# Performance work log

Measured on AMD Instinct MI355X. Metric: run time of the kernel, lower is better.

Reference implementation:

```python
import jax, jax.numpy as jnp
import numpy as np

B, S, N, F, H, G, O, P = 32, 12, 2048, 1, 128, 64, 1, 3


def setup_inputs() -> dict:
    key = jax.random.key(0)
    ks = jax.random.split(key, 12)
    x = jax.random.normal(ks[0], (B, S, N, F), jnp.float32)
    # row-normalized random adjacency (dense, as the module uses a dense adj)
    adj = jax.random.uniform(ks[1], (N, N), jnp.float32)
    adj = adj / jnp.sum(adj, axis=1, keepdims=True)
    s = 0.05
    return {
        "x": x,
        "adj": adj,
        "W_g1": jax.random.normal(ks[2], (F, G), jnp.float32) * s,
        "b_g1": jnp.zeros((G,), jnp.float32),
        "W_g2": jax.random.normal(ks[3], (G, H), jnp.float32) * s,
        "b_g2": jnp.zeros((H,), jnp.float32),
        "W_ih": jax.random.normal(ks[4], (H, 3 * H), jnp.float32) * s,
        "W_hh": jax.random.normal(ks[5], (H, 3 * H), jnp.float32) * s,
        "b_ih": jnp.zeros((3 * H,), jnp.float32),
        "b_hh": jnp.zeros((3 * H,), jnp.float32),
        "W_fc": jax.random.normal(ks[6], (H, O), jnp.float32) * s,
        "b_fc": jnp.zeros((O,), jnp.float32),
        "pred_len": P,
    }


def _tgcn_cell(xt, h, adj, W_g1, b_g1, W_g2, b_g2, W_ih, W_hh, b_ih, b_hh):
    # 2-layer GCN: relu(A X W1 + b1) -> A H1 W2 + b2
    # compute X@W first (F, G small), then propagate with dense adj
    h1 = jax.nn.relu(jnp.einsum('mn,bng->bmg', adj, xt @ W_g1) + b_g1)  # (B,N,G)
    xg = jnp.einsum('mn,bnh->bmh', adj, h1 @ W_g2) + b_g2              # (B,N,H)
    # standard GRU cell (gate order r, z, n)
    gx = xg @ W_ih + b_ih                                              # (B,N,3H)
    gh = h @ W_hh + b_hh
    rx, zx, nx = jnp.split(gx, 3, axis=-1)
    rh, zh, nh = jnp.split(gh, 3, axis=-1)
    r = jax.nn.sigmoid(rx + rh)
    z = jax.nn.sigmoid(zx + zh)
    n = jnp.tanh(nx + r * nh)
    return (1.0 - z) * n + z * h


def reference(x, adj, W_g1, b_g1, W_g2, b_g2, W_ih, W_hh, b_ih, b_hh, W_fc, b_fc, pred_len):
    cell = lambda h, xt: _tgcn_cell(xt, h, adj, W_g1, b_g1, W_g2, b_g2,
                                    W_ih, W_hh, b_ih, b_hh)
    h0 = jnp.zeros((x.shape[0], x.shape[2], W_hh.shape[0]), x.dtype)
    # encoder: sequential over seq_len
    h, _ = jax.lax.scan(lambda h, xt: (cell(h, xt), None),
                        h0, jnp.moveaxis(x, 1, 0))
    def pstep(h, _):
        out = h @ W_fc + b_fc          # (B,N,O)
        h = cell(h, out)
        return h, out
    _, preds = jax.lax.scan(pstep, h, None, length=pred_len)
    return jnp.moveaxis(preds, 0, 1)   # (B, pred_len, N, O)
```

## Files before the change

### kernel.cpp

```cpp
#include <hip/hip_runtime.h>
#include <math.h>

#define NB 32
#define SS 12
#define NN 2048
#define HH 128
#define GG 64
#define PP 3
#define RR (NN*NB)

typedef __attribute__((ext_vector_type(8))) _Float16 half8;
typedef __attribute__((ext_vector_type(4))) float f32x4;

__device__ __forceinline__ void glds16(const void* g, const void* l) {
    __builtin_amdgcn_global_load_lds(
        (const __attribute__((address_space(1))) void*)g,
        (__attribute__((address_space(3))) void*)l, 16, 0, 0);
}

#define DRAIN_STAGING() asm volatile("s_waitcnt vmcnt(0) lgkmcnt(0)" ::: "memory")

#define RAWBAR() __builtin_amdgcn_s_barrier()
#define LGKM0() do { asm volatile("s_waitcnt lgkmcnt(0)" ::: "memory"); \
                     __builtin_amdgcn_sched_barrier(0); } while (0)
#define VMW(n)  do { asm volatile("s_waitcnt vmcnt(" #n ")" ::: "memory"); \
                     __builtin_amdgcn_sched_barrier(0); } while (0)

__global__ __launch_bounds__(256) void cvtadj(
    const float* __restrict__ src, _Float16* __restrict__ dst)
{
    size_t i0 = ((size_t)blockIdx.x * 256 + threadIdx.x) * 8;
    float4 v0 = *(const float4*)(src + i0);
    float4 v1 = *(const float4*)(src + i0 + 4);
    union { _Float16 h[8]; uint4 q; } H;
    H.h[0]=(_Float16)v0.x; H.h[1]=(_Float16)v0.y;
    H.h[2]=(_Float16)v0.z; H.h[3]=(_Float16)v0.w;
    H.h[4]=(_Float16)v1.x; H.h[5]=(_Float16)v1.y;
    H.h[6]=(_Float16)v1.z; H.h[7]=(_Float16)v1.w;
    *(uint4*)(dst + i0) = H.q;
}

__global__ __launch_bounds__(256) void xcvt_enc(
    const float* __restrict__ x, _Float16* __restrict__ dst)
{
    const int row = blockIdx.x;
    const int t = row >> 5, b = row & 31;
    const size_t n0 = (size_t)threadIdx.x * 8;
    const float* src = x + ((size_t)b*SS + t)*NN;
    float4 v0 = *(const float4*)(src + n0);
    float4 v1 = *(const float4*)(src + n0 + 4);
    union { _Float16 h[8]; uint4 q; } H;
    H.h[0]=(_Float16)v0.x; H.h[1]=(_Float16)v0.y;
    H.h[2]=(_Float16)v0.z; H.h[3]=(_Float16)v0.w;
    H.h[4]=(_Float16)v1.x; H.h[5]=(_Float16)v1.y;
    H.h[6]=(_Float16)v1.z; H.h[7]=(_Float16)v1.w;
    *(uint4*)(dst + (size_t)row*NN + n0) = H.q;
}

__global__ __launch_bounds__(256) void wprep(
    const float* __restrict__ Wg2, const float* __restrict__ Wih,
    const float* __restrict__ bih, const float* __restrict__ bg2,
    float* __restrict__ Wc, float* __restrict__ bc)
{
    int idx = blockIdx.x * 256 + threadIdx.x;
    if (idx < GG*384) {
        int g = idx / 384, o = idx % 384;
        float s = 0.f;
        for (int k = 0; k < HH; ++k)
            s = fmaf(Wg2[g*HH + k], Wih[k*384 + o], s);
        Wc[idx] = s;
    } else if (idx < GG*384 + 384) {
        int o = idx - GG*384;
        float s = bih[o];
        for (int k = 0; k < HH; ++k)
            s = fmaf(bg2[k], Wih[k*384 + o], s);
        bc[o] = s;
    }
}

__global__ __launch_bounds__(256) void wprep2(
    const float* __restrict__ Wc, const float* __restrict__ Whh,
    _Float16* __restrict__ Wcomb)
{
    int idx = blockIdx.x * 256 + threadIdx.x;
    if (idx < 384*192) {
        int o = idx / 192, k = idx % 192;
        float v = (k < 64) ? Wc[k*384 + o] : Whh[(k-64)*384 + o];
        Wcomb[idx] = (_Float16)v;
    }
}

__global__ __launch_bounds__(256) void h1T(
    const float* __restrict__ axpart, int col_base, size_t part_stride,
    const float* __restrict__ Wg1, const float* __restrict__ bg1,
    _Float16* __restrict__ Hh)
{
    const int c = blockIdx.x;
    const int ty = blockIdx.y;
    const int b = c >> 6, g = c & 63;
    const float w1 = Wg1[g], b1 = bg1[g];
    const size_t n0 = (size_t)threadIdx.x * 8;
    const size_t rowoff = (size_t)(col_base + ty*32 + b) * NN + n0;
    float f[8] = {0,0,0,0,0,0,0,0};
#pragma unroll
    for (int p = 0; p < 2; ++p) {
        const float4* q = (const float4*)(axpart + p*part_stride + rowoff);
        float4 v0 = q[0], v1 = q[1];
        f[0]+=v0.x; f[1]+=v0.y; f[2]+=v0.z; f[3]+=v0.w;
        f[4]+=v1.x; f[5]+=v1.y; f[6]+=v1.z; f[7]+=v1.w;
    }
    union { _Float16 h[8]; uint4 q; } H;
#pragma unroll
    for (int k = 0; k < 8; ++k)
        H.h[k] = (_Float16)fmaxf(fmaf(f[k], w1, b1), 0.f);
    *(uint4*)(Hh + ((size_t)ty*2048 + c) * NN + n0) = H.q;
}

__global__ __launch_bounds__(512, 2) void gemm384(
    const _Float16* __restrict__ Ah, const _Float16* __restrict__ Bh,
    _Float16* __restrict__ C, int ldc, int kchunk)
{
    __shared__ __align__(16) _Float16 As[3][8192];
    __shared__ __align__(16) _Float16 Bs[3][12288];
    const int tid = threadIdx.x;
    const int w = tid >> 6, lane = tid & 63;
    const int lm = lane & 15, lq = lane >> 4;
    const int wm = w >> 2, wn = w & 3;
    const int wg = blockIdx.x;
    const int m0 = (wg & 7) * 256, n0 = (wg >> 3) * 384;
    const int NT = kchunk >> 5;

    f32x4 acc[8][6];
#pragma unroll
    for (int i = 0; i < 8; ++i)
#pragma unroll
        for (int j = 0; j < 6; ++j) acc[i][j] = (f32x4){0.f,0.f,0.f,0.f};

    auto stA = [&](int buf, int T) {
#pragma unroll
        for (int c = 0; c < 2; ++c) {
            int chunk = w*2 + c;
            glds16(Ah + (size_t)(m0 + chunk*16 + lm)*2048 + T*32 + lq*8,
                   &As[buf][chunk*512]);
        }
    };
    auto stB = [&](int buf, int T) {
#pragma unroll
        for (int c = 0; c < 3; ++c) {
            int chunk = w*3 + c;
            glds16(Bh + (size_t)(n0 + chunk*16 + lm)*2048 + T*32 + lq*8,
                   &Bs[buf][chunk*512]);
        }
    };

    stA(0, 0); stB(0, 0);
    stA(1, 1); stB(1, 1);
    VMW(5);
    RAWBAR();

    int cur = 0;
    for (int T = 0; T < NT; ++T) {
        const int b2 = (cur >= 1) ? cur - 1 : 2;
        half8 af[4], bf[6];
#pragma unroll
        for (int i = 0; i < 4; ++i)
            af[i] = *(const half8*)&As[cur][(wm*8 + i)*512 + lane*8];
#pragma unroll
        for (int j = 0; j < 6; ++j)
            bf[j] = *(const half8*)&Bs[cur][(wn*6 + j)*512 + lane*8];
        if (T + 2 < NT) stA(b2, T + 2);
        __builtin_amdgcn_s_setprio(1);
#pragma unroll
        for (int i = 0; i < 4; ++i)
#pragma unroll
            for (int j = 0; j < 6; ++j)
                acc[i][j] = __builtin_amdgcn_mfma_f32_16x16x32_f16(
                    af[i], bf[j], acc[i][j], 0, 0, 0);
        __builtin_amdgcn_s_setprio(0);
#pragma unroll
        for (int i = 0; i < 4; ++i)
            af[i] = *(const half8*)&As[cur][(wm*8 + 4 + i)*512 + lane*8];
        if (T + 2 < NT) stB(b2, T + 2);
        __builtin_amdgcn_s_setprio(1);
#pragma unroll
        for (int i = 0; i < 4; ++i)
#pragma unroll
            for (int j = 0; j < 6; ++j)
                acc[4 + i][j] = __builtin_amdgcn_mfma_f32_16x16x32_f16(
                    af[i], bf[j], acc[4 + i][j], 0, 0, 0);
        __builtin_amdgcn_s_setprio(0);
        if (T + 2 < NT)      { VMW(5); }
        else if (T + 1 < NT) { VMW(0); }
        RAWBAR();
        cur = (cur < 2) ? cur + 1 : 0;
    }
#pragma unroll
    for (int i = 0; i < 8; ++i) {
        int row = m0 + wm*128 + i*16 + lq*4;
#pragma unroll
        for (int j = 0; j < 6; ++j) {
            int col = n0 + wn*96 + j*16 + lm;
            _Float16* cp = C + (size_t)row*ldc + col;
            cp[0*(size_t)ldc] = (_Float16)acc[i][j][0];
            cp[1*(size_t)ldc] = (_Float16)acc[i][j][1];
            cp[2*(size_t)ldc] = (_Float16)acc[i][j][2];
            cp[3*(size_t)ldc] = (_Float16)acc[i][j][3];
        }
    }
}

#define GEMM_BODY                                                              \
    __shared__ __align__(16) _Float16 As[8192];    \
    __shared__ __align__(16) _Float16 Bs[8192];                                \
    const int tid  = threadIdx.x;                                              \
    const int wv   = tid >> 6, lane = tid & 63;                                \
    const int lm   = lane & 15, lq = lane >> 4;                                \
    const int m0   = blockIdx.y * 128;                                         \
    const int n0   = blockIdx.x * 128;                                         \
    const int wm   = wv >> 1, wn = wv & 1;                                     \
    f32x4 acc[4][4];                                                           \
    _Pragma("unroll")                                                          \
    for (int i = 0; i < 4; ++i)                                                \
        _Pragma("unroll")                                                      \
        for (int j = 0; j < 4; ++j) acc[i][j] = (f32x4){0.f,0.f,0.f,0.f};      \
    const int kbeg = blockIdx.z * kchunk, kend = kbeg + kchunk;                \
    for (int k0 = kbeg; k0 < kend; k0 += 64) {                                 \
        _Pragma("unroll")                                                      \
        for (int t = 0; t < 4; ++t) {                                          \
            int tt = wv*4 + t;                                                 \
            int rt = tt >> 1, kt = tt & 1;                                     \
            glds16(Ah + (size_t)(m0 + rt*16 + lm)*2048 + k0 + kt*32 + lq*8,    \
                   &As[tt*512]);                                               \
            glds16(Bh + (size_t)(n0 + rt*16 + lm)*2048 + k0 + kt*32 + lq*8,    \
                   &Bs[tt*512]);                                               \
        }                                                                      \
        DRAIN_STAGING();                                                       \
        __syncthreads();                                                       \
        _Pragma("unroll")                                                      \
        for (int ks = 0; ks < 2; ++ks) {                                       \
            half8 af[4], bf[4];                                                \
            _Pragma("unroll")                                                  \
            for (int i = 0; i < 4; ++i) {                                      \
                af[i] = *(const half8*)&As[((wm*4 + i)*2 + ks)*512 + lane*8];  \
                bf[i] = *(const half8*)&Bs[((wn*4 + i)*2 + ks)*512 + lane*8];  \
            }                                                                  \
            _Pragma("unroll")                                                  \
            for (int i = 0; i < 4; ++i)                                        \
                _Pragma("unroll")                                              \
                for (int j = 0; j < 4; ++j)                                    \
                    acc[i][j] = __builtin_amdgcn_mfma_f32_16x16x32_f16(        \
                        af[i], bf[j], acc[i][j], 0, 0, 0);                     \
        }                                                                      \
        __syncthreads();                                                       \
    }

__global__ __launch_bounds__(256) void gemm_mfma_p(
    const _Float16* __restrict__ Ah, const _Float16* __restrict__ Bh,
    float* __restrict__ Cbase, int kchunk, size_t partstride)
{
    float* C = Cbase + (size_t)blockIdx.z * partstride;
    GEMM_BODY
#pragma unroll
    for (int i = 0; i < 4; ++i) {
        int row = m0 + wm*64 + i*16 + lq*4;
#pragma unroll
        for (int j = 0; j < 4; ++j) {
            int col = n0 + wn*64 + j*16 + lm;
            float* cp = C + (size_t)row*2048 + col;
            cp[0*2048] = acc[i][j][0];
            cp[1*2048] = acc[i][j][1];
            cp[2*2048] = acc[i][j][2];
            cp[3*2048] = acc[i][j][3];
        }
    }
}

__global__ __launch_bounds__(256) void gemm_mfma_T(
    const _Float16* __restrict__ Ah, const _Float16* __restrict__ Bh,
    float* __restrict__ Cbase, int kchunk, size_t partstride)
{
    float* C = Cbase + (size_t)blockIdx.z * partstride;
    GEMM_BODY
#pragma unroll
    for (int i = 0; i < 4; ++i) {
        int row = m0 + wm*64 + i*16 + lq*4;
#pragma unroll
        for (int j = 0; j < 4; ++j) {
            int col = n0 + wn*64 + j*16 + lm;
            float4 v = {acc[i][j][0], acc[i][j][1], acc[i][j][2], acc[i][j][3]};
            *(float4*)(C + (size_t)col*2048 + row) = v;
        }
    }
}

__global__ __launch_bounds__(256) void zsum(
    const float* __restrict__ p0, const float* __restrict__ p1,
    _Float16* __restrict__ z)
{
    size_t i0 = ((size_t)blockIdx.x * 256 + threadIdx.x) * 8;
    float4 a0 = *(const float4*)(p0 + i0), a1 = *(const float4*)(p0 + i0 + 4);
    float4 b0 = *(const float4*)(p1 + i0), b1 = *(const float4*)(p1 + i0 + 4);
    union { _Float16 h[8]; uint4 q; } H;
    H.h[0]=(_Float16)(a0.x+b0.x); H.h[1]=(_Float16)(a0.y+b0.y);
    H.h[2]=(_Float16)(a0.z+b0.z); H.h[3]=(_Float16)(a0.w+b0.w);
    H.h[4]=(_Float16)(a1.x+b1.x); H.h[5]=(_Float16)(a1.y+b1.y);
    H.h[6]=(_Float16)(a1.z+b1.z); H.h[7]=(_Float16)(a1.w+b1.w);
    *(uint4*)(z + i0) = H.q;
}

__device__ __forceinline__ float sigmoidf_(float x) {
    return __builtin_amdgcn_rcpf(1.f + __expf(-x));
}
__device__ __forceinline__ float tanhf_(float x) {
    float xc = fmaxf(-15.f, fminf(15.f, x));
    float e = __expf(-2.f * xc);
    return (1.f - e) * __builtin_amdgcn_rcpf(1.f + e);
}

template<int HZERO>
__global__ __launch_bounds__(512, 2) void gatemm2(
    const _Float16* __restrict__ Z16, int ldz, int zoff,
    const _Float16* __restrict__ Wcomb,
    const float* __restrict__ bc, const float* __restrict__ bhh,
    _Float16* __restrict__ H16)
{
    const int tid = threadIdx.x;
    const int w = tid >> 6, lane = tid & 63;
    const int lm = lane & 15, lq = lane >> 4;
    const int o0 = w*16 + lq*4;

    half8 wr[6], wz[6], wn[6];
#pragma unroll
    for (int c = 0; c < 6; ++c) {
        wr[c] = *(const half8*)&Wcomb[(size_t)((w     )*16 + lm)*192 + c*32 + lq*8];
        wz[c] = *(const half8*)&Wcomb[(size_t)((8 + w )*16 + lm)*192 + c*32 + lq*8];
        wn[c] = *(const half8*)&Wcomb[(size_t)((16 + w)*16 + lm)*192 + c*32 + lq*8];
    }
    float br_[4], bz_[4], bnx_[4], bnh_[4];
#pragma unroll
    for (int reg = 0; reg < 4; ++reg) {
        int o = o0 + reg;
        br_[reg]  = bc[o]     + bhh[o];
        bz_[reg]  = bc[o+128] + bhh[o+128];
        bnx_[reg] = bc[o+256];
        bnh_[reg] = bhh[o+256];
    }

    const int g0 = blockIdx.x * 8;

    auto zp_of = [&](int g, int rt2) {
        int r = g*32 + rt2*16 + lm;
        return (const half8*)&Z16[(size_t)(r >> 5)*ldz + zoff + (r & 31)*64 + lq*8];
    };

    half8 zA[2][2], zB[2][2];
#pragma unroll
    for (int rt2 = 0; rt2 < 2; ++rt2) {
        const half8* zp = zp_of(g0, rt2);
        zA[rt2][0] = zp[0]; zA[rt2][1] = zp[4];
    }

    union HU { ushort4 q; _Float16 h[4]; };

#pragma unroll
    for (int i = 0; i < 8; ++i) {
        const int g = g0 + i;
        const int r0 = g*32;

        half8 hf[2][4];
        HU holdu[2];
        if (!HZERO) {
#pragma unroll
            for (int rt2 = 0; rt2 < 2; ++rt2) {
                const _Float16* hp = &H16[(size_t)(r0 + rt2*16 + lm)*128];
#pragma unroll
                for (int c4 = 0; c4 < 4; ++c4)
                    hf[rt2][c4] = *(const half8*)(hp + c4*32 + lq*8);
                holdu[rt2].q = *(const ushort4*)(hp + o0);
            }
        }

        f32x4 ar[2], az[2], anx[2], anh[2];
#pragma unroll
        for (int rt2 = 0; rt2 < 2; ++rt2) {
            ar[rt2]  = (f32x4){0.f,0.f,0.f,0.f};
            az[rt2]  = (f32x4){0.f,0.f,0.f,0.f};
            anx[rt2] = (f32x4){0.f,0.f,0.f,0.f};
            anh[rt2] = (f32x4){0.f,0.f,0.f,0.f};
        }
#pragma unroll
        for (int rt2 = 0; rt2 < 2; ++rt2) {
#pragma unroll
            for (int c2 = 0; c2 < 2; ++c2) {
                half8 rf = (i & 1) ? zB[rt2][c2] : zA[rt2][c2];
                ar[rt2]  = __builtin_amdgcn_mfma_f32_16x16x32_f16(
                    wr[c2], rf, ar[rt2], 0, 0, 0);
                az[rt2]  = __builtin_amdgcn_mfma_f32_16x16x32_f16(
                    wz[c2], rf, az[rt2], 0, 0, 0);
                anx[rt2] = __builtin_amdgcn_mfma_f32_16x16x32_f16(
                    wn[c2], rf, anx[rt2], 0, 0, 0);
            }
            if (!HZERO) {
#pragma unroll
                for (int c4 = 0; c4 < 4; ++c4) {
                    ar[rt2]  = __builtin_amdgcn_mfma_f32_16x16x32_f16(
                        wr[2+c4], hf[rt2][c4], ar[rt2], 0, 0, 0);
                    az[rt2]  = __builtin_amdgcn_mfma_f32_16x16x32_f16(
                        wz[2+c4], hf[rt2][c4], az[rt2], 0, 0, 0);
                    anh[rt2] = __builtin_amdgcn_mfma_f32_16x16x32_f16(
                        wn[2+c4], hf[rt2][c4], anh[rt2], 0, 0, 0);
                }
            }
        }
        if (i + 1 < 8) {
#pragma unroll
            for (int rt2 = 0; rt2 < 2; ++rt2) {
                const half8* zp = zp_of(g + 1, rt2);
                if (i & 1) { zA[rt2][0] = zp[0]; zA[rt2][1] = zp[4]; }
                else       { zB[rt2][0] = zp[0]; zB[rt2][1] = zp[4]; }
            }
        }
        if (!HZERO) {
            RAWBAR();
            __builtin_amdgcn_sched_barrier(0);
        }

#pragma unroll
        for (int rt2 = 0; rt2 < 2; ++rt2) {
            const int r = r0 + rt2*16 + lm;
            HU outu;
#pragma unroll
            for (int reg = 0; reg < 4; ++reg) {
                float hold = HZERO ? 0.f : (float)holdu[rt2].h[reg];
                float rg = sigmoidf_(ar[rt2][reg] + br_[reg]);
                float zg = sigmoidf_(az[rt2][reg] + bz_[reg]);
                float ng = tanhf_(anx[rt2][reg] + bnx_[reg]
                                  + rg*(anh[rt2][reg] + bnh_[reg]));
                outu.h[reg] = (_Float16)((1.f - zg)*ng + zg*hold);
            }
            *(ushort4*)&H16[(size_t)r*128 + o0] = outu.q;
        }
    }
}

__global__ __launch_bounds__(512, 2) void grufuse(
    const _Float16* __restrict__ Z16,
    const _Float16* __restrict__ Wcomb,
    const float* __restrict__ bc, const float* __restrict__ bhh,
    _Float16* __restrict__ H16)
{
    __shared__ __align__(16) _Float16 Hl[8192];
    const int tid = threadIdx.x;
    const int w = tid >> 6, lane = tid & 63;
    const int lm = lane & 15, lq = lane >> 4;
    const int o0 = w*16 + lq*4;
    const int blk = blockIdx.x;

    half8 wr[6], wz[6], wn[6];
#pragma unroll
    for (int c = 0; c < 6; ++c) {
        wr[c] = *(const half8*)&Wcomb[(size_t)((w     )*16 + lm)*192 + c*32 + lq*8];
        wz[c] = *(const half8*)&Wcomb[(size_t)((8 + w )*16 + lm)*192 + c*32 + lq*8];
        wn[c] = *(const half8*)&Wcomb[(size_t)((16 + w)*16 + lm)*192 + c*32 + lq*8];
    }
    float br_[4], bz_[4], bnx_[4], bnh_[4];
#pragma unroll
    for (int reg = 0; reg < 4; ++reg) {
        int o = o0 + reg;
        br_[reg]  = bc[o]     + bhh[o];
        bz_[reg]  = bc[o+128] + bhh[o+128];
        bnx_[reg] = bc[o+256];
        bnh_[reg] = bhh[o+256];
    }

    int zrow[2], hrd[2], hmsk[2], hwr[2];
#pragma unroll
    for (int rt2 = 0; rt2 < 2; ++rt2) {
        const int lr = rt2*16 + lm;
        zrow[rt2] = blk*24576 + lr*64 + lq*8;
        hrd[rt2]  = lr*256 + lq*16;
        hmsk[rt2] = (lr & 7) << 4;
        hwr[rt2]  = (lr*256 + o0*2) ^ hmsk[rt2];
    }

    union HU { ushort4 q; _Float16 h[4]; };
    HU hold[2];
    hold[0].q = (ushort4){0,0,0,0};
    hold[1].q = (ushort4){0,0,0,0};

    half8 zA[2][2], zB[2][2];
#pragma unroll
    for (int rt2 = 0; rt2 < 2; ++rt2)
#pragma unroll
        for (int c2 = 0; c2 < 2; ++c2) {
            zA[rt2][c2] = *(const half8*)&Z16[(size_t)(zrow[rt2] + c2*32)];
            zB[rt2][c2] = *(const half8*)&Z16[(size_t)(zrow[rt2] + 2048 + c2*32)];
        }

    {
        f32x4 ar[2], az[2], anx[2];
#pragma unroll
        for (int rt2 = 0; rt2 < 2; ++rt2) {
            ar[rt2] = (f32x4){0.f,0.f,0.f,0.f};
            az[rt2] = (f32x4){0.f,0.f,0.f,0.f};
            anx[rt2] = (f32x4){0.f,0.f,0.f,0.f};
#pragma unroll
            for (int c2 = 0; c2 < 2; ++c2) {
                ar[rt2]  = __builtin_amdgcn_mfma_f32_16x16x32_f16(
                    wr[c2], zA[rt2][c2], ar[rt2], 0, 0, 0);
                az[rt2]  = __builtin_amdgcn_mfma_f32_16x16x32_f16(
                    wz[c2], zA[rt2][c2], az[rt2], 0, 0, 0);
                anx[rt2] = __builtin_amdgcn_mfma_f32_16x16x32_f16(
                    wn[c2], zA[rt2][c2], anx[rt2], 0, 0, 0);
            }
        }
#pragma unroll
        for (int rt2 = 0; rt2 < 2; ++rt2) {
            HU outu;
#pragma unroll
            for (int reg = 0; reg < 4; ++reg) {
                float rg = sigmoidf_(ar[rt2][reg] + br_[reg]);
                float zg = sigmoidf_(az[rt2][reg] + bz_[reg]);
                float ng = tanhf_(anx[rt2][reg] + bnx_[reg] + rg*bnh_[reg]);
                outu.h[reg] = (_Float16)((1.f - zg)*ng);
            }
            hold[rt2] = outu;
            *(ushort4*)((char*)Hl + hwr[rt2]) = outu.q;
        }
        LGKM0();
        RAWBAR();
    }

#pragma unroll
    for (int t = 1; t < SS; ++t) {
        const int rb = ((t & 1) ^ 1) * 8192;
        const int wb = (t & 1) * 8192;
        half8 hf[2][4];
#pragma unroll
        for (int rt2 = 0; rt2 < 2; ++rt2)
#pragma unroll
            for (int c4 = 0; c4 < 4; ++c4)
                hf[rt2][c4] = *(const half8*)((const char*)Hl + rb
                    + ((hrd[rt2] + c4*64) ^ hmsk[rt2]));

        f32x4 ar[2], az[2], anx[2], anh[2];
#pragma unroll
        for (int rt2 = 0; rt2 < 2; ++rt2) {
            ar[rt2]  = (f32x4){0.f,0.f,0.f,0.f};
            az[rt2]  = (f32x4){0.f,0.f,0.f,0.f};
            anx[rt2] = (f32x4){0.f,0.f,0.f,0.f};
            anh[rt2] = (f32x4){0.f,0.f,0.f,0.f};
#pragma unroll
            for (int c2 = 0; c2 < 2; ++c2) {
                half8 rf = (t & 1) ? zB[rt2][c2] : zA[rt2][c2];
                ar[rt2]  = __builtin_amdgcn_mfma_f32_16x16x32_f16(
                    wr[c2], rf, ar[rt2], 0, 0, 0);
                az[rt2]  = __builtin_amdgcn_mfma_f32_16x16x32_f16(
                    wz[c2], rf, az[rt2], 0, 0, 0);
                anx[rt2] = __builtin_amdgcn_mfma_f32_16x16x32_f16(
                    wn[c2], rf, anx[rt2], 0, 0, 0);
            }
#pragma unroll
            for (int c4 = 0; c4 < 4; ++c4) {
                ar[rt2]  = __builtin_amdgcn_mfma_f32_16x16x32_f16(
                    wr[2+c4], hf[rt2][c4], ar[rt2], 0, 0, 0);
                az[rt2]  = __builtin_amdgcn_mfma_f32_16x16x32_f16(
                    wz[2+c4], hf[rt2][c4], az[rt2], 0, 0, 0);
                anh[rt2] = __builtin_amdgcn_mfma_f32_16x16x32_f16(
                    wn[2+c4], hf[rt2][c4], anh[rt2], 0, 0, 0);
            }
        }
        if (t + 1 < SS) {
#pragma unroll
            for (int rt2 = 0; rt2 < 2; ++rt2)
#pragma unroll
                for (int c2 = 0; c2 < 2; ++c2) {
                    const half8* zp = (const half8*)
                        &Z16[(size_t)(zrow[rt2] + (t+1)*2048 + c2*32)];
                    if (t & 1) zA[rt2][c2] = *zp;
                    else       zB[rt2][c2] = *zp;
                }
        }

#pragma unroll
        for (int rt2 = 0; rt2 < 2; ++rt2) {
            HU outu;
#pragma unroll
            for (int reg = 0; reg < 4; ++reg) {
                float hv = (float)hold[rt2].h[reg];
                float rg = sigmoidf_(ar[rt2][reg] + br_[reg]);
                float zg = sigmoidf_(az[rt2][reg] + bz_[reg]);
                float ng = tanhf_(anx[rt2][reg] + bnx_[reg]
                                  + rg*(anh[rt2][reg] + bnh_[reg]));
                outu.h[reg] = (_Float16)((1.f - zg)*ng + zg*hv);
            }
            hold[rt2] = outu;
            if (t < SS-1)
                *(ushort4*)((char*)Hl + wb + hwr[rt2]) = outu.q;
        }
        if (t < SS-1) {
            LGKM0();
            RAWBAR();
        }
    }

#pragma unroll
    for (int rt2 = 0; rt2 < 2; ++rt2)
        *(ushort4*)&H16[(size_t)(blk*32 + rt2*16 + lm)*128 + o0] = hold[rt2].q;
}

__global__ __launch_bounds__(256) void fck(
    const _Float16* __restrict__ h,
    const float* __restrict__ Wfc, const float* __restrict__ bfc,
    float* __restrict__ out_p,
    _Float16* __restrict__ Xdh)
{
    int w = (blockIdx.x * 256 + threadIdx.x) >> 6;
    int lane = threadIdx.x & 63;
    const _Float16* hr = h + (size_t)w*HH + lane*2;
    const float2* wf = (const float2*)Wfc;
    float2 b2 = wf[lane];
    float s = (float)hr[0]*b2.x + (float)hr[1]*b2.y;
#pragma unroll
    for (int off = 32; off; off >>= 1) s += __shfl_xor(s, off);
    if (lane == 0) {
        s += bfc[0];
        int n = w >> 5, b = w & 31;
        out_p[(size_t)b*(PP*NN) + n] = s;
        Xdh[(size_t)b*NN + n] = (_Float16)s;
    }
}

extern "C" void kernel_launch(void* const* d_in, const int* in_sizes, int n_in,
                              void* d_out, int out_size, void* d_ws, size_t ws_size,
                              hipStream_t stream)
{
    const float* x    = (const float*)d_in[0];
    const float* adj  = (const float*)d_in[1];
    const float* Wg1  = (const float*)d_in[2];
    const float* bg1  = (const float*)d_in[3];
    const float* Wg2  = (const float*)d_in[4];
    const float* bg2  = (const float*)d_in[5];
    const float* Wih  = (const float*)d_in[6];
    const float* Whh  = (const float*)d_in[7];
    const float* bih  = (const float*)d_in[8];
    const float* bhh  = (const float*)d_in[9];
    const float* Wfc  = (const float*)d_in[10];
    const float* bfc  = (const float*)d_in[11];

    float* ws = (float*)d_ws;
    float* Wc   = ws;
    float* bc   = Wc + GG*384;
    float* AXe  = bc + 1024;
    float* AXd  = AXe + (size_t)2*384*NN;
    _Float16* Ah    = (_Float16*)(AXd + (size_t)2*128*NN);
    _Float16* Xeh   = Ah    + (size_t)NN*NN;
    _Float16* Xdh   = Xeh   + (size_t)384*NN;
    _Float16* Hgh   = Xdh   + (size_t)128*NN;
    _Float16* Z16   = Hgh   + (size_t)12288*NN;
    _Float16* H16   = Z16   + (size_t)NN*24576;
    _Float16* Wcomb = H16   + (size_t)RR*HH;
    float* Zp = (float*)(Hgh + (size_t)2048*NN);

    {
        size_t used = (size_t)((char*)(Wcomb + (size_t)384*192) - (char*)d_ws);
        hipMemsetAsync(d_ws, 0, used, stream);
    }

    cvtadj<<<2048, 256, 0, stream>>>(adj, Ah);
    wprep<<<98, 256, 0, stream>>>(Wg2, Wih, bih, bg2, Wc, bc);
    wprep2<<<288, 256, 0, stream>>>(Wc, Whh, Wcomb);
    xcvt_enc<<<384, 256, 0, stream>>>(x, Xeh);
    gemm_mfma_T<<<dim3(3, 16, 2), 256, 0, stream>>>(
        Ah, Xeh, AXe, 1024, (size_t)384*NN);

    float* outp = (float*)d_out;

    for (int g = 0; g < 2; ++g) {
        h1T<<<dim3(NN, 6), 256, 0, stream>>>(
            AXe, g*192, (size_t)384*NN, Wg1, bg1, Hgh);
        gemm384<<<256, 512, 0, stream>>>(
            Ah, Hgh, Z16 + (size_t)g*12288, 24576, 2048);
    }
    grufuse<<<RR/32, 512, 0, stream>>>(Z16, Wcomb, bc, bhh, H16);

    for (int p = 0; p < PP; ++p) {
        fck<<<RR/4, 256, 0, stream>>>(H16, Wfc, bfc, outp + (size_t)p*NN, Xdh);
        if (p < PP-1) {
            gemm_mfma_T<<<dim3(1, 16, 2), 256, 0, stream>>>(
                Ah, Xdh, AXd, 1024, (size_t)128*NN);
            h1T<<<dim3(NN, 1), 256, 0, stream>>>(
                AXd, 0, (size_t)128*NN, Wg1, bg1, Hgh);
            gemm_mfma_p<<<dim3(16, 16, 2), 256, 0, stream>>>(
                Ah, Hgh, Zp, 1024, (size_t)NN*NN);
            zsum<<<2048, 256, 0, stream>>>(Zp, Zp + (size_t)NN*NN, Z16);
            gatemm2<0><<<256, 512, 0, stream>>>(
                Z16, 2048, 0, Wcomb, bc, bhh, H16);
        }
    }
}
```

Measured before the change: 850.1 us.

## Replace split-K decoder GEMM plus zsum with pipelined full-K fp16 GEMM

```diff
diff --git a/kernel.cpp b/kernel.cpp
--- a/kernel.cpp
+++ b/kernel.cpp
@@ -93,7 +93,7 @@
 __global__ __launch_bounds__(256) void h1T(
     const float* __restrict__ axpart, int col_base, size_t part_stride,
     const float* __restrict__ Wg1, const float* __restrict__ bg1,
-    _Float16* __restrict__ Hh)
+    _Float16* __restrict__ Hh, int np)
 {
     const int c = blockIdx.x;
     const int ty = blockIdx.y;
@@ -102,8 +102,7 @@
     const size_t n0 = (size_t)threadIdx.x * 8;
     const size_t rowoff = (size_t)(col_base + ty*32 + b) * NN + n0;
     float f[8] = {0,0,0,0,0,0,0,0};
-#pragma unroll
-    for (int p = 0; p < 2; ++p) {
+    for (int p = 0; p < np; ++p) {
         const float4* q = (const float4*)(axpart + p*part_stride + rowoff);
         float4 v0 = q[0], v1 = q[1];
         f[0]+=v0.x; f[1]+=v0.y; f[2]+=v0.z; f[3]+=v0.w;
@@ -200,6 +199,98 @@
 #pragma unroll
         for (int j = 0; j < 6; ++j) {
             int col = n0 + wn*96 + j*16 + lm;
+            _Float16* cp = C + (size_t)row*ldc + col;
+            cp[0*(size_t)ldc] = (_Float16)acc[i][j][0];
+            cp[1*(size_t)ldc] = (_Float16)acc[i][j][1];
+            cp[2*(size_t)ldc] = (_Float16)acc[i][j][2];
+            cp[3*(size_t)ldc] = (_Float16)acc[i][j][3];
+        }
+    }
+}
+
+__global__ __launch_bounds__(256, 2) void gemmdz(
+    const _Float16* __restrict__ Ah, const _Float16* __restrict__ Bh,
+    _Float16* __restrict__ C, int ldc)
+{
+    __shared__ __align__(16) _Float16 As[3][4096];
+    __shared__ __align__(16) _Float16 Bs[3][4096];
+    const int tid = threadIdx.x;
+    const int w = tid >> 6, lane = tid & 63;
+    const int lm = lane & 15, lq = lane >> 4;
+    const int wm = w >> 1, wn = w & 1;
+    const int m0 = blockIdx.y * 128, n0 = blockIdx.x * 128;
+    const int NT = 2048 >> 5;
+
+    f32x4 acc[4][4];
+#pragma unroll
+    for (int i = 0; i < 4; ++i)
+#pragma unroll
+        for (int j = 0; j < 4; ++j) acc[i][j] = (f32x4){0.f,0.f,0.f,0.f};
+
+    auto stA = [&](int buf, int T) {
+#pragma unroll
+        for (int c = 0; c < 2; ++c) {
+            int chunk = w*2 + c;
+            glds16(Ah + (size_t)(m0 + chunk*16 + lm)*2048 + T*32 + lq*8,
+                   &As[buf][chunk*512]);
+        }
+    };
+    auto stB = [&](int buf, int T) {
+#pragma unroll
+        for (int c = 0; c < 2; ++c) {
+            int chunk = w*2 + c;
+            glds16(Bh + (size_t)(n0 + chunk*16 + lm)*2048 + T*32 + lq*8,
+                   &Bs[buf][chunk*512]);
+        }
+    };
+
+    stA(0, 0); stB(0, 0);
+    stA(1, 1); stB(1, 1);
+    VMW(4);
+    RAWBAR();
+
+    int cur = 0;
+    for (int T = 0; T < NT; ++T) {
+        const int b2 = (cur >= 1) ? cur - 1 : 2;
+        half8 af[2], bf[4];
+#pragma unroll
+        for (int i = 0; i < 2; ++i)
+            af[i] = *(const half8*)&As[cur][(wm*4 + i)*512 + lane*8];
+#pragma unroll
+        for (int j = 0; j < 4; ++j)
+            bf[j] = *(const half8*)&Bs[cur][(wn*4 + j)*512 + lane*8];
+        if (T + 2 < NT) stA(b2, T + 2);
+        __builtin_amdgcn_s_setprio(1);
+#pragma unroll
+        for (int i = 0; i < 2; ++i)
+#pragma unroll
+            for (int j = 0; j < 4; ++j)
+                acc[i][j] = __builtin_amdgcn_mfma_f32_16x16x32_f16(
+                    af[i], bf[j], acc[i][j], 0, 0, 0);
+        __builtin_amdgcn_s_setprio(0);
+#pragma unroll
+        for (int i = 0; i < 2; ++i)
+            af[i] = *(const half8*)&As[cur][(wm*4 + 2 + i)*512 + lane*8];
+        if (T + 2 < NT) stB(b2, T + 2);
+        __builtin_amdgcn_s_setprio(1);
+#pragma unroll
+        for (int i = 0; i < 2; ++i)
+#pragma unroll
+            for (int j = 0; j < 4; ++j)
+                acc[2 + i][j] = __builtin_amdgcn_mfma_f32_16x16x32_f16(
+                    af[i], bf[j], acc[2 + i][j], 0, 0, 0);
+        __builtin_amdgcn_s_setprio(0);
+        if (T + 2 < NT)      { VMW(4); }
+        else if (T + 1 < NT) { VMW(0); }
+        RAWBAR();
+        cur = (cur < 2) ? cur + 1 : 0;
+    }
+#pragma unroll
+    for (int i = 0; i < 4; ++i) {
+        int row = m0 + wm*64 + i*16 + lq*4;
+#pragma unroll
+        for (int j = 0; j < 4; ++j) {
+            int col = n0 + wn*64 + j*16 + lm;
             _Float16* cp = C + (size_t)row*ldc + col;
             cp[0*(size_t)ldc] = (_Float16)acc[i][j][0];
             cp[1*(size_t)ldc] = (_Float16)acc[i][j][1];
@@ -254,27 +345,6 @@
         __syncthreads();                                                       \
     }
 
-__global__ __launch_bounds__(256) void gemm_mfma_p(
-    const _Float16* __restrict__ Ah, const _Float16* __restrict__ Bh,
-    float* __restrict__ Cbase, int kchunk, size_t partstride)
-{
-    float* C = Cbase + (size_t)blockIdx.z * partstride;
-    GEMM_BODY
-#pragma unroll
-    for (int i = 0; i < 4; ++i) {
-        int row = m0 + wm*64 + i*16 + lq*4;
-#pragma unroll
-        for (int j = 0; j < 4; ++j) {
-            int col = n0 + wn*64 + j*16 + lm;
-            float* cp = C + (size_t)row*2048 + col;
-            cp[0*2048] = acc[i][j][0];
-            cp[1*2048] = acc[i][j][1];
-            cp[2*2048] = acc[i][j][2];
-            cp[3*2048] = acc[i][j][3];
-        }
-    }
-}
-
 __global__ __launch_bounds__(256) void gemm_mfma_T(
     const _Float16* __restrict__ Ah, const _Float16* __restrict__ Bh,
     float* __restrict__ Cbase, int kchunk, size_t partstride)
@@ -291,21 +361,6 @@
             *(float4*)(C + (size_t)col*2048 + row) = v;
         }
     }
-}
-
-__global__ __launch_bounds__(256) void zsum(
-    const float* __restrict__ p0, const float* __restrict__ p1,
-    _Float16* __restrict__ z)
-{
-    size_t i0 = ((size_t)blockIdx.x * 256 + threadIdx.x) * 8;
-    float4 a0 = *(const float4*)(p0 + i0), a1 = *(const float4*)(p0 + i0 + 4);
-    float4 b0 = *(const float4*)(p1 + i0), b1 = *(const float4*)(p1 + i0 + 4);
-    union { _Float16 h[8]; uint4 q; } H;
-    H.h[0]=(_Float16)(a0.x+b0.x); H.h[1]=(_Float16)(a0.y+b0.y);
-    H.h[2]=(_Float16)(a0.z+b0.z); H.h[3]=(_Float16)(a0.w+b0.w);
-    H.h[4]=(_Float16)(a1.x+b1.x); H.h[5]=(_Float16)(a1.y+b1.y);
-    H.h[6]=(_Float16)(a1.z+b1.z); H.h[7]=(_Float16)(a1.w+b1.w);
-    *(uint4*)(z + i0) = H.q;
 }
 
 __device__ __forceinline__ float sigmoidf_(float x) {
@@ -660,7 +715,7 @@
     _Float16* Z16   = Hgh   + (size_t)12288*NN;
     _Float16* H16   = Z16   + (size_t)NN*24576;
     _Float16* Wcomb = H16   + (size_t)RR*HH;
-    float* Zp = (float*)(Hgh + (size_t)2048*NN);
+    float* AXd8 = AXe;
 
     {
         size_t used = (size_t)((char*)(Wcomb + (size_t)384*192) - (char*)d_ws);
@@ -678,7 +733,7 @@
 
     for (int g = 0; g < 2; ++g) {
         h1T<<<dim3(NN, 6), 256, 0, stream>>>(
-            AXe, g*192, (size_t)384*NN, Wg1, bg1, Hgh);
+            AXe, g*192, (size_t)384*NN, Wg1, bg1, Hgh, 2);
         gemm384<<<256, 512, 0, stream>>>(
             Ah, Hgh, Z16 + (size_t)g*12288, 24576, 2048);
     }
@@ -687,13 +742,11 @@
     for (int p = 0; p < PP; ++p) {
         fck<<<RR/4, 256, 0, stream>>>(H16, Wfc, bfc, outp + (size_t)p*NN, Xdh);
         if (p < PP-1) {
-            gemm_mfma_T<<<dim3(1, 16, 2), 256, 0, stream>>>(
-                Ah, Xdh, AXd, 1024, (size_t)128*NN);
+            gemm_mfma_T<<<dim3(1, 16, 8), 256, 0, stream>>>(
+                Ah, Xdh, AXd8, 256, (size_t)128*NN);
             h1T<<<dim3(NN, 1), 256, 0, stream>>>(
-                AXd, 0, (size_t)128*NN, Wg1, bg1, Hgh);
-            gemm_mfma_p<<<dim3(16, 16, 2), 256, 0, stream>>>(
-                Ah, Hgh, Zp, 1024, (size_t)NN*NN);
-            zsum<<<2048, 256, 0, stream>>>(Zp, Zp + (size_t)NN*NN, Z16);
+                AXd8, 0, (size_t)128*NN, Wg1, bg1, Hgh, 8);
+            gemmdz<<<dim3(16, 16), 256, 0, stream>>>(Ah, Hgh, Z16, 2048);
             gatemm2<0><<<256, 512, 0, stream>>>(
                 Z16, 2048, 0, Wcomb, bc, bhh, H16);
         }
```

New measurement: 842.7 us. Within noise of the previous version (-0.9%).
